# Kernel optimization log

Hardware: AMD Instinct MI355X
Metric: run time of the kernel (lower is better)

The kernel has to match this reference:

```python
import jax, jax.numpy as jnp
import numpy as np

NUM_REL = 7
EPS = 1e-5
N, E = 30000, 480000
D_IN, D_H = 21, 512


def _bn(x, g, b):
    # BatchNorm1d over nodes (training-mode batch statistics, biased var like torch)
    mu = x.mean(axis=0)
    var = x.var(axis=0)
    return (x - mu) * jax.lax.rsqrt(var + EPS) * g + b


def _conv(x, src, seg_idx, lin_w, lin_b, self_w, self_b, bn_g, bn_b):
    # GeometricRelationalGraphConv: gather src features, scatter-add per (dst, relation)
    d = x.shape[1]
    msg = x[src]                                                   # (E, d)
    upd = jax.ops.segment_sum(msg, seg_idx, num_segments=N * NUM_REL)
    upd = upd.reshape(N, NUM_REL * d)                              # (N, 7*d)
    out = upd @ lin_w.T + lin_b + x @ self_w.T + self_b            # linear + self-loop
    out = _bn(out, bn_g, bn_b)                                     # conv-internal BN
    return jax.nn.relu(out)


def setup_inputs() -> dict:
    key = jax.random.key(0)
    ks = jax.random.split(key, 16)
    inp = {
        "x": jax.random.normal(ks[0], (N, D_IN), dtype=jnp.float32),
        "src": jax.random.randint(ks[1], (E,), 0, N, dtype=jnp.int32),
        "dst": jax.random.randint(ks[2], (E,), 0, N, dtype=jnp.int32),
        "rel": jax.random.randint(ks[3], (E,), 0, NUM_REL, dtype=jnp.int32),
    }
    dims = [(D_IN, D_H), (D_H, D_H), (D_H, D_H)]
    k = 4
    for i, (din, dout) in enumerate(dims):
        inp[f"lin_w{i}"] = jax.random.normal(ks[k], (dout, NUM_REL * din), dtype=jnp.float32) * 0.05
        inp[f"self_w{i}"] = jax.random.normal(ks[k + 1], (dout, din), dtype=jnp.float32) * 0.05
        k += 2
        inp[f"lin_b{i}"] = jnp.zeros((dout,), jnp.float32)
        inp[f"self_b{i}"] = jnp.zeros((dout,), jnp.float32)
        inp[f"bn1_g{i}"] = jnp.ones((dout,), jnp.float32)
        inp[f"bn1_b{i}"] = jnp.zeros((dout,), jnp.float32)
        inp[f"bn2_g{i}"] = jnp.ones((dout,), jnp.float32)
        inp[f"bn2_b{i}"] = jnp.zeros((dout,), jnp.float32)
    return inp


def reference(x, src, dst, rel,
              lin_w0, lin_b0, self_w0, self_b0, bn1_g0, bn1_b0, bn2_g0, bn2_b0,
              lin_w1, lin_b1, self_w1, self_b1, bn1_g1, bn1_b1, bn2_g1, bn2_b1,
              lin_w2, lin_b2, self_w2, self_b2, bn1_g2, bn1_b2, bn2_g2, bn2_b2):
    seg_idx = dst * NUM_REL + rel                                  # (E,)
    layers = [
        (lin_w0, lin_b0, self_w0, self_b0, bn1_g0, bn1_b0, bn2_g0, bn2_b0),
        (lin_w1, lin_b1, self_w1, self_b1, bn1_g1, bn1_b1, bn2_g1, bn2_b1),
        (lin_w2, lin_b2, self_w2, self_b2, bn1_g2, bn1_b2, bn2_g2, bn2_b2),
    ]
    hiddens = []
    h = x
    for lw, lb, sw, sb, g1, b1, g2, b2 in layers:
        h = _conv(h, src, seg_idx, lw, lb, sw, sb, g1, b1)
        h = _bn(h, g2, b2)                                         # GearNet outer BN
        hiddens.append(h)
    return jnp.concatenate(hiddens, axis=-1)                      # (N, 3*512) concat_hidden
```

## Files before the change

### kernel.cpp

```cpp
#include <hip/hip_runtime.h>

#define NN   30000
#define NE   480000
#define NR   7
#define NSEG (NN*NR)
#define DH   512
#define DIN  21
#define EPSB 1e-5f
#define BK   32
#define KSEG 3584
#define CHMAX 15360

typedef __attribute__((ext_vector_type(8))) short bf16x8;
typedef __attribute__((ext_vector_type(8))) unsigned short u16x8;
typedef __attribute__((ext_vector_type(4))) float f32x4;
typedef unsigned short ushortT;

static inline size_t align256(size_t x){ return (x + 255) & ~(size_t)255; }

__device__ inline float bf2f(ushortT u){
    unsigned int i = ((unsigned int)u) << 16; float f; __builtin_memcpy(&f, &i, 4); return f;
}
__device__ inline ushortT f2bf(float f){
    unsigned int i; __builtin_memcpy(&i, &f, 4);
    unsigned int r = i + 0x7FFFu + ((i >> 16) & 1u);
    return (ushortT)(r >> 16);
}

__device__ inline void load_lds16(const ushortT* g, ushortT* l){
    __builtin_amdgcn_global_load_lds((const __attribute__((address_space(1))) unsigned int*)g,
                                     (__attribute__((address_space(3))) unsigned int*)l,
                                     16, 0, 0);
}


__global__ void hist_k(const int* __restrict__ dst, const int* __restrict__ rel,
                       int* __restrict__ counts){
    int e = blockIdx.x*256 + threadIdx.x;
    if (e < NE) atomicAdd(&counts[dst[e]*NR + rel[e]], 1);
}

__global__ void scan1_k(const int* __restrict__ counts, int* __restrict__ bsum){
    __shared__ int sd[256];
    int t = threadIdx.x;
    int base = blockIdx.x*1024 + t*4;
    int s = 0;
#pragma unroll
    for (int i = 0; i < 4; i++){ int idx = base + i; if (idx < NSEG) s += counts[idx]; }
    sd[t] = s; __syncthreads();
    for (int off = 128; off > 0; off >>= 1){
        if (t < off) sd[t] += sd[t+off];
        __syncthreads();
    }
    if (t == 0) bsum[blockIdx.x] = sd[0];
}

__global__ void scan2_k(int* __restrict__ bsum, int nb, int* __restrict__ seg_start){
    __shared__ int sd[256];
    int t = threadIdx.x;
    int v = (t < nb) ? bsum[t] : 0;
    sd[t] = v; __syncthreads();
    for (int off = 1; off < 256; off <<= 1){
        int x = sd[t];
        if (t >= off) x += sd[t-off];
        __syncthreads();
        sd[t] = x; __syncthreads();
    }
    if (t < nb) bsum[t] = (t == 0) ? 0 : sd[t-1];
    if (t == 0) seg_start[NSEG] = NE;
}

__global__ void scan3_k(const int* __restrict__ counts, const int* __restrict__ bsum,
                        int* __restrict__ seg_start){
    __shared__ int sd[256];
    int t = threadIdx.x;
    int base = blockIdx.x*1024 + t*4;
    int v[4]; int s = 0;
#pragma unroll
    for (int i = 0; i < 4; i++){ int idx = base + i; v[i] = (idx < NSEG) ? counts[idx] : 0; s += v[i]; }
    sd[t] = s; __syncthreads();
    for (int off = 1; off < 256; off <<= 1){
        int x = sd[t];
        if (t >= off) x += sd[t-off];
        __syncthreads();
        sd[t] = x; __syncthreads();
    }
    int excl = sd[t] - s + bsum[blockIdx.x];
#pragma unroll
    for (int i = 0; i < 4; i++){
        int idx = base + i;
        if (idx < NSEG){ seg_start[idx] = excl; excl += v[i]; }
    }
}

__global__ void scatter_k(const int* __restrict__ src, const int* __restrict__ dst,
                          const int* __restrict__ rel, const int* __restrict__ seg_start,
                          int* __restrict__ cursor, int* __restrict__ src_sorted){
    int e = blockIdx.x*256 + threadIdx.x;
    if (e < NE){
        int s = dst[e]*NR + rel[e];
        int pos = seg_start[s] + atomicAdd(&cursor[s], 1);
        src_sorted[pos] = src[e];
    }
}


__global__ void segsum21b_k(const float* __restrict__ x0,
                            const int* __restrict__ seg_start, const int* __restrict__ src_sorted,
                            ushortT* __restrict__ Acat){
    int n = blockIdx.x;
    int t = threadIdx.x;
    ushortT* arow = Acat + (long)n*192;
    if (t < DIN){
        int sb = n*NR;
        int e0 = seg_start[sb];
#pragma unroll
        for (int r = 0; r < NR; r++){
            int e1 = seg_start[sb + r + 1];
            float a = 0.f;
            for (int e = e0; e < e1; e++) a += x0[(long)src_sorted[e]*DIN + t];
            e0 = e1;
            arow[r*DIN + t] = f2bf(a);
        }
        arow[7*DIN + t] = f2bf(x0[(long)n*DIN + t]);
    }
    if (t >= 40) arow[168 + (t - 40)] = 0;
}


__global__ __launch_bounds__(256)
void segsum_wave_k(const ushortT* __restrict__ hbf,
                   const int* __restrict__ seg_start, const int* __restrict__ src_sorted,
                   ushortT* __restrict__ Acat, int c0, int cn){
    int wid = (blockIdx.x*256 + threadIdx.x) >> 6;
    if (wid >= cn) return;
    const int n = c0 + wid;
    const int lane = (threadIdx.x & 63);
    const int co = lane*8;

    int sb[8];
#pragma unroll
    for (int i = 0; i < 8; i++) sb[i] = seg_start[n*NR + i];

    ushortT* arow = Acat + (long)wid*KSEG + co;
#pragma unroll
    for (int r = 0; r < NR; r++){
        float a[8];
#pragma unroll
        for (int j = 0; j < 8; j++) a[j] = 0.f;
        int e = sb[r], e1 = sb[r+1];
        for (; e + 1 < e1; e += 2){
            u16x8 v0 = *reinterpret_cast<const u16x8*>(hbf + (long)src_sorted[e]*DH + co);
            u16x8 v1 = *reinterpret_cast<const u16x8*>(hbf + (long)src_sorted[e+1]*DH + co);
#pragma unroll
            for (int j = 0; j < 8; j++) a[j] += bf2f((ushortT)v0[j]) + bf2f((ushortT)v1[j]);
        }
        if (e < e1){
            u16x8 v = *reinterpret_cast<const u16x8*>(hbf + (long)src_sorted[e]*DH + co);
#pragma unroll
            for (int j = 0; j < 8; j++) a[j] += bf2f((ushortT)v[j]);
        }
        u16x8 o;
#pragma unroll
        for (int j = 0; j < 8; j++) o[j] = f2bf(a[j]);
        *reinterpret_cast<u16x8*>(arow + r*DH) = o;
    }
}


__global__ void convw_k(const float* __restrict__ lw, const float* __restrict__ sw,
                        int d, int Kp, ushortT* __restrict__ Wc){
    int i = blockIdx.x*256 + threadIdx.x;
    if (i < DH*Kp){
        int n = i / Kp, k = i % Kp;
        float v;
        if (k < 7*d)      v = lw[(long)n*7*d + k];
        else if (k < 8*d) v = sw[(long)n*d + (k - 7*d)];
        else              v = 0.f;
        Wc[i] = f2bf(v);
    }
}


__global__ __launch_bounds__(256)
void gemm_mfma_k(const ushortT* __restrict__ A, int lda, int ntA,
                 const ushortT* __restrict__ hbase, int M,
                 const ushortT* __restrict__ W, int ldw,
                 const float* __restrict__ b1, const float* __restrict__ b2,
                 float* __restrict__ C, int nt, float* __restrict__ sums){
    __shared__ ushortT As[3][128*BK];
    __shared__ ushortT Bs[3][128*BK];
    const int t    = threadIdx.x;

    const int nwg = gridDim.x;
    int q = nwg >> 3, rmd = nwg & 7;
    int xcd = blockIdx.x & 7, slot = blockIdx.x >> 3;
    int l = xcd*q + min(xcd, rmd) + slot;
    const int bm = (l >> 2)*128;
    const int bn = (l & 3)*128;

    const int w    = t >> 6;
    const int lane = t & 63;

    int f0 = w*128 + lane, f1 = f0 + 64;
    const int ar0 = min(bm + (f0 >> 2), M-1), ac0 = (f0 & 3)*8;
    const int ar1 = min(bm + (f1 >> 2), M-1), ac1 = (f1 & 3)*8;
    const int br0 = bn + (f0 >> 2), br1 = bn + (f1 >> 2);
    const int d0 = (w*128 +  0)*8;
    const int d1 = (w*128 + 64)*8;

    f32x4 acc[4][4];
#pragma unroll
    for (int m = 0; m < 4; m++)
#pragma unroll
        for (int n = 0; n < 4; n++) acc[m][n] = (f32x4){0.f,0.f,0.f,0.f};

    const int wm = w >> 1, wn = w & 1;
    const int r = lane & 15, hi = lane >> 4;

    auto stage = [&](int kt, int b){
        const ushortT* p0;
        const ushortT* p1;
        if (kt < ntA){
            p0 = A + (long)ar0*lda + kt*BK + ac0;
            p1 = A + (long)ar1*lda + kt*BK + ac1;
        } else {
            int k0 = (kt - ntA)*BK;
            p0 = hbase + (long)ar0*DH + k0 + ac0;
            p1 = hbase + (long)ar1*DH + k0 + ac1;
        }
        load_lds16(p0, &As[b][d0]);
        load_lds16(p1, &As[b][d1]);
        load_lds16(W + (long)br0*ldw + kt*BK + ac0, &Bs[b][d0]);
        load_lds16(W + (long)br1*ldw + kt*BK + ac1, &Bs[b][d1]);
    };

    stage(0, 0);
    stage(1, 1);

    for (int kt = 0; kt < nt; ++kt){
        if (kt + 1 < nt) asm volatile("s_waitcnt vmcnt(4)" ::: "memory");
        else             asm volatile("s_waitcnt vmcnt(0)" ::: "memory");
        __builtin_amdgcn_s_barrier();
        __builtin_amdgcn_sched_barrier(0);
        if (kt + 2 < nt) stage(kt + 2, (kt + 2) % 3);
        const int buf = kt % 3;
        bf16x8 af[4], bfr[4];
#pragma unroll
        for (int m = 0; m < 4; m++)
            af[m] = *reinterpret_cast<const bf16x8*>(&As[buf][(wm*64 + m*16 + r)*BK + hi*8]);
#pragma unroll
        for (int n = 0; n < 4; n++)
            bfr[n] = *reinterpret_cast<const bf16x8*>(&Bs[buf][(wn*64 + n*16 + r)*BK + hi*8]);
#pragma unroll
        for (int m = 0; m < 4; m++)
#pragma unroll
            for (int n = 0; n < 4; n++)
                acc[m][n] = __builtin_amdgcn_mfma_f32_16x16x32_bf16(af[m], bfr[n], acc[m][n], 0, 0, 0);
    }

#pragma unroll
    for (int n = 0; n < 4; n++){
        int col = bn + wn*64 + n*16 + r;
        float bb = b1[col] + b2[col];
        float s = 0.f, s2 = 0.f;
#pragma unroll
        for (int m = 0; m < 4; m++){
            int row = bm + wm*64 + m*16 + hi*4;
#pragma unroll
            for (int q2 = 0; q2 < 4; q2++){
                if (row + q2 < M){
                    float v = acc[m][n][q2] + bb;
                    C[(long)(row + q2)*DH + col] = v;
                    s += v; s2 = fmaf(v, v, s2);
                }
            }
        }
        s  += __shfl_xor(s, 16);  s  += __shfl_xor(s, 32);
        s2 += __shfl_xor(s2, 16); s2 += __shfl_xor(s2, 32);
        if (hi == 0){
            atomicAdd(&sums[col], s);
            atomicAdd(&sums[DH + col], s2);
        }
    }
}


__global__ void finalize_k(const float* __restrict__ sums, const float* __restrict__ g,
                           const float* __restrict__ b, float* __restrict__ ac){
    int c = blockIdx.x*256 + threadIdx.x;
    if (c < DH){
        float mu  = sums[c] * (1.f/NN);
        float var = sums[DH + c] * (1.f/NN) - mu*mu;
        var = fmaxf(var, 0.f);
        float a = g[c] * rsqrtf(var + EPSB);
        ac[c]      = a;
        ac[DH + c] = fmaf(-mu, a, b[c]);
    }
}

__global__ void bnrelu_k(float* __restrict__ buf, int M, const float* __restrict__ ac,
                         float* __restrict__ sums2){
    int col = blockIdx.x*256 + threadIdx.x;
    int r0 = blockIdx.y*128;
    int r1 = min(r0 + 128, M);
    float a = ac[col], c = ac[DH + col];
    float s = 0.f, s2 = 0.f;
    for (int r = r0; r < r1; r++){
        long idx = (long)r*DH + col;
        float y = fmaxf(fmaf(a, buf[idx], c), 0.f);
        buf[idx] = y;
        s += y; s2 = fmaf(y, y, s2);
    }
    atomicAdd(&sums2[col], s);
    atomicAdd(&sums2[DH + col], s2);
}

__global__ void bn2write_k(const float* __restrict__ buf, const float* __restrict__ ac,
                           float* __restrict__ out, ushortT* __restrict__ hbf, int layer){
    long i = (long)blockIdx.x*256 + threadIdx.x;
    if (i < (long)NN*DH){
        int r = (int)(i >> 9);
        int c = (int)(i & 511);
        float h = fmaf(ac[c], buf[i], ac[DH + c]);
        out[(long)r*(3*DH) + layer*DH + c] = h;
        hbf[i] = f2bf(h);
    }
}


extern "C" void kernel_launch(void* const* d_in, const int* in_sizes, int n_in,
                              void* d_out, int out_size, void* d_ws, size_t ws_size,
                              hipStream_t stream){
    const float* x0  = (const float*)d_in[0];
    const int*   src = (const int*)d_in[1];
    const int*   dst = (const int*)d_in[2];
    const int*   rel = (const int*)d_in[3];
    const float* lin_w[3]  = {(const float*)d_in[4],  (const float*)d_in[12], (const float*)d_in[20]};
    const float* self_w[3] = {(const float*)d_in[5],  (const float*)d_in[13], (const float*)d_in[21]};
    const float* lin_b[3]  = {(const float*)d_in[6],  (const float*)d_in[14], (const float*)d_in[22]};
    const float* self_b[3] = {(const float*)d_in[7],  (const float*)d_in[15], (const float*)d_in[23]};
    const float* bn1_g[3]  = {(const float*)d_in[8],  (const float*)d_in[16], (const float*)d_in[24]};
    const float* bn1_b[3]  = {(const float*)d_in[9],  (const float*)d_in[17], (const float*)d_in[25]};
    const float* bn2_g[3]  = {(const float*)d_in[10], (const float*)d_in[18], (const float*)d_in[26]};
    const float* bn2_b[3]  = {(const float*)d_in[11], (const float*)d_in[19], (const float*)d_in[27]};

    char* ws = (char*)d_ws;
    size_t off = 0;
    auto alloc = [&](size_t bytes)->char*{ char* p = ws + off; off = align256(off + bytes); return p; };

    int*     counts     = (int*)alloc((size_t)NSEG*4);
    int*     cursor     = (int*)alloc((size_t)NSEG*4);
    int*     seg_start  = (int*)alloc((size_t)(NSEG+1)*4);
    int*     bsum       = (int*)alloc(1024*4);
    int*     src_sorted = (int*)alloc((size_t)NE*4);
    float*   stats      = (float*)alloc((size_t)8*DH*4);
    float*   sums1 = stats;            float* sums2 = stats + 2*DH;
    float*   ac1   = stats + 4*DH;     float* ac2   = stats + 6*DH;
    float*   outbuf = (float*)alloc((size_t)NN*DH*4);
    ushortT* hbf    = (ushortT*)alloc((size_t)NN*DH*2);
    ushortT* Wcat   = (ushortT*)alloc((size_t)DH*4096*2);
    ushortT* Acat0  = (ushortT*)alloc((size_t)NN*192*2);

    size_t remain = (ws_size > off) ? (ws_size - off) : 0;
    long max_nodes = (long)(remain / ((size_t)KSEG*2));
    int chunk = (int)((max_nodes > CHMAX) ? CHMAX : max_nodes);
    chunk &= ~127;
    if (chunk < 128) chunk = 128;
    ushortT* Acat = (ushortT*)(ws + off);

    hipMemsetAsync(counts, 0, (size_t)NSEG*4, stream);
    hipMemsetAsync(cursor, 0, (size_t)NSEG*4, stream);
    hist_k<<<(NE+255)/256, 256, 0, stream>>>(dst, rel, counts);
    int nb = (NSEG + 1023)/1024;
    scan1_k<<<nb, 256, 0, stream>>>(counts, bsum);
    scan2_k<<<1, 256, 0, stream>>>(bsum, nb, seg_start);
    scan3_k<<<nb, 256, 0, stream>>>(counts, bsum, seg_start);
    scatter_k<<<(NE+255)/256, 256, 0, stream>>>(src, dst, rel, seg_start, cursor, src_sorted);

    const int MB = (NN + 127)/128;

    for (int layer = 0; layer < 3; layer++){
        int d  = (layer == 0) ? DIN : DH;
        int Kp = (layer == 0) ? 192 : 8*DH;
        convw_k<<<(DH*Kp + 255)/256, 256, 0, stream>>>(lin_w[layer], self_w[layer], d, Kp, Wcat);
        hipMemsetAsync(stats, 0, (size_t)4*DH*4, stream);

        if (layer == 0){
            segsum21b_k<<<NN, 64, 0, stream>>>(x0, seg_start, src_sorted, Acat0);
            gemm_mfma_k<<<MB*4, 256, 0, stream>>>(
                Acat0, 192, 6, Acat0, NN, Wcat, 192,
                lin_b[layer], self_b[layer], outbuf, 6, sums1);
        } else {
            for (int c0 = 0; c0 < NN; c0 += chunk){
                int cn = (NN - c0 < chunk) ? (NN - c0) : chunk;
                segsum_wave_k<<<(cn + 3)/4, 256, 0, stream>>>(
                    hbf, seg_start, src_sorted, Acat, c0, cn);
                gemm_mfma_k<<<((cn + 127)/128)*4, 256, 0, stream>>>(
                    Acat, KSEG, 112, hbf + (long)c0*DH, cn, Wcat, 4096,
                    lin_b[layer], self_b[layer],
                    outbuf + (long)c0*DH, 128, sums1);
            }
        }

        finalize_k<<<2, 256, 0, stream>>>(sums1, bn1_g[layer], bn1_b[layer], ac1);
        bnrelu_k<<<dim3(2, (NN+127)/128), 256, 0, stream>>>(outbuf, NN, ac1, sums2);
        finalize_k<<<2, 256, 0, stream>>>(sums2, bn2_g[layer], bn2_b[layer], ac2);
        bn2write_k<<<((long)NN*DH + 255)/256, 256, 0, stream>>>(outbuf, ac2, (float*)d_out, hbf, layer);
    }
}
```

Baseline: 959.5 us.

## Overlap next-chunk segment sum with GEMM in a merged kernel, narrow GEMM tile

```diff
diff --git a/kernel.cpp b/kernel.cpp
--- a/kernel.cpp
+++ b/kernel.cpp
@@ -128,43 +128,54 @@
 }
 
 
+__device__ inline void segsum_body(const ushortT* __restrict__ hbf,
+                                   const int* __restrict__ seg_start,
+                                   const int* __restrict__ src_sorted,
+                                   ushortT* __restrict__ Acat,
+                                   int wid, int c0, int lane){
+    const int n = c0 + wid;
+    const int co = lane*8;
+
+    int sb[8];
+#pragma unroll
+    for (int i = 0; i < 8; i++) sb[i] = seg_start[n*NR + i];
+
+    ushortT* arow = Acat + (long)wid*KSEG + co;
+#pragma unroll
+    for (int r = 0; r < NR; r++){
+        float a[8];
+#pragma unroll
+        for (int j = 0; j < 8; j++) a[j] = 0.f;
+        int e = sb[r], e1 = sb[r+1];
+        for (; e + 3 < e1; e += 4){
+            u16x8 v0 = *reinterpret_cast<const u16x8*>(hbf + (long)src_sorted[e  ]*DH + co);
+            u16x8 v1 = *reinterpret_cast<const u16x8*>(hbf + (long)src_sorted[e+1]*DH + co);
+            u16x8 v2 = *reinterpret_cast<const u16x8*>(hbf + (long)src_sorted[e+2]*DH + co);
+            u16x8 v3 = *reinterpret_cast<const u16x8*>(hbf + (long)src_sorted[e+3]*DH + co);
+#pragma unroll
+            for (int j = 0; j < 8; j++)
+                a[j] += (bf2f((ushortT)v0[j]) + bf2f((ushortT)v1[j]))
+                      + (bf2f((ushortT)v2[j]) + bf2f((ushortT)v3[j]));
+        }
+        for (; e < e1; e++){
+            u16x8 v = *reinterpret_cast<const u16x8*>(hbf + (long)src_sorted[e]*DH + co);
+#pragma unroll
+            for (int j = 0; j < 8; j++) a[j] += bf2f((ushortT)v[j]);
+        }
+        u16x8 o;
+#pragma unroll
+        for (int j = 0; j < 8; j++) o[j] = f2bf(a[j]);
+        *reinterpret_cast<u16x8*>(arow + r*DH) = o;
+    }
+}
+
 __global__ __launch_bounds__(256)
 void segsum_wave_k(const ushortT* __restrict__ hbf,
                    const int* __restrict__ seg_start, const int* __restrict__ src_sorted,
                    ushortT* __restrict__ Acat, int c0, int cn){
     int wid = (blockIdx.x*256 + threadIdx.x) >> 6;
     if (wid >= cn) return;
-    const int n = c0 + wid;
-    const int lane = (threadIdx.x & 63);
-    const int co = lane*8;
-
-    int sb[8];
-#pragma unroll
-    for (int i = 0; i < 8; i++) sb[i] = seg_start[n*NR + i];
-
-    ushortT* arow = Acat + (long)wid*KSEG + co;
-#pragma unroll
-    for (int r = 0; r < NR; r++){
-        float a[8];
-#pragma unroll
-        for (int j = 0; j < 8; j++) a[j] = 0.f;
-        int e = sb[r], e1 = sb[r+1];
-        for (; e + 1 < e1; e += 2){
-            u16x8 v0 = *reinterpret_cast<const u16x8*>(hbf + (long)src_sorted[e]*DH + co);
-            u16x8 v1 = *reinterpret_cast<const u16x8*>(hbf + (long)src_sorted[e+1]*DH + co);
-#pragma unroll
-            for (int j = 0; j < 8; j++) a[j] += bf2f((ushortT)v0[j]) + bf2f((ushortT)v1[j]);
-        }
-        if (e < e1){
-            u16x8 v = *reinterpret_cast<const u16x8*>(hbf + (long)src_sorted[e]*DH + co);
-#pragma unroll
-            for (int j = 0; j < 8; j++) a[j] += bf2f((ushortT)v[j]);
-        }
-        u16x8 o;
-#pragma unroll
-        for (int j = 0; j < 8; j++) o[j] = f2bf(a[j]);
-        *reinterpret_cast<u16x8*>(arow + r*DH) = o;
-    }
+    segsum_body(hbf, seg_start, src_sorted, Acat, wid, c0, threadIdx.x & 63);
 }
 
 
@@ -183,38 +194,46 @@
 
 
 __global__ __launch_bounds__(256)
-void gemm_mfma_k(const ushortT* __restrict__ A, int lda, int ntA,
-                 const ushortT* __restrict__ hbase, int M,
-                 const ushortT* __restrict__ W, int ldw,
-                 const float* __restrict__ b1, const float* __restrict__ b2,
-                 float* __restrict__ C, int nt, float* __restrict__ sums){
+void gemm_seg_k(int gemmBlocks,
+                const ushortT* __restrict__ A, int lda, int ntA,
+                const ushortT* __restrict__ hbase, int M,
+                const ushortT* __restrict__ W, int ldw,
+                const float* __restrict__ b1, const float* __restrict__ b2,
+                float* __restrict__ C, int nt, float* __restrict__ sums,
+                const ushortT* __restrict__ hbf,
+                const int* __restrict__ seg_start, const int* __restrict__ src_sorted,
+                ushortT* __restrict__ Acat2, int nc0, int ncn){
     __shared__ ushortT As[3][128*BK];
-    __shared__ ushortT Bs[3][128*BK];
-    const int t    = threadIdx.x;
-
-    const int nwg = gridDim.x;
+    __shared__ ushortT Bs[3][ 64*BK];
+    const int t = threadIdx.x;
+
+    if ((int)blockIdx.x >= gemmBlocks){
+        int wid = ((int)blockIdx.x - gemmBlocks)*4 + (t >> 6);
+        if (wid < ncn)
+            segsum_body(hbf, seg_start, src_sorted, Acat2, wid, nc0, t & 63);
+        return;
+    }
+
+    const int nwg = gemmBlocks;
     int q = nwg >> 3, rmd = nwg & 7;
     int xcd = blockIdx.x & 7, slot = blockIdx.x >> 3;
     int l = xcd*q + min(xcd, rmd) + slot;
-    const int bm = (l >> 2)*128;
-    const int bn = (l & 3)*128;
-
-    const int w    = t >> 6;
+    const int bm = (l >> 3)*128;
+    const int bn = (l & 7)*64;
+
+    const int ar0 = min(bm + (t >> 2), M-1);
+    const int ar1 = min(bm + 64 + (t >> 2), M-1);
+    const int acu = (t & 3)*8;
+    const int brw = bn + (t >> 2);
+
+    f32x4 acc[4][2];
+#pragma unroll
+    for (int m = 0; m < 4; m++)
+#pragma unroll
+        for (int n = 0; n < 2; n++) acc[m][n] = (f32x4){0.f,0.f,0.f,0.f};
+
+    const int w = t >> 6;
     const int lane = t & 63;
-
-    int f0 = w*128 + lane, f1 = f0 + 64;
-    const int ar0 = min(bm + (f0 >> 2), M-1), ac0 = (f0 & 3)*8;
-    const int ar1 = min(bm + (f1 >> 2), M-1), ac1 = (f1 & 3)*8;
-    const int br0 = bn + (f0 >> 2), br1 = bn + (f1 >> 2);
-    const int d0 = (w*128 +  0)*8;
-    const int d1 = (w*128 + 64)*8;
-
-    f32x4 acc[4][4];
-#pragma unroll
-    for (int m = 0; m < 4; m++)
-#pragma unroll
-        for (int n = 0; n < 4; n++) acc[m][n] = (f32x4){0.f,0.f,0.f,0.f};
-
     const int wm = w >> 1, wn = w & 1;
     const int r = lane & 15, hi = lane >> 4;
 
@@ -222,46 +241,45 @@
         const ushortT* p0;
         const ushortT* p1;
         if (kt < ntA){
-            p0 = A + (long)ar0*lda + kt*BK + ac0;
-            p1 = A + (long)ar1*lda + kt*BK + ac1;
+            p0 = A + (long)ar0*lda + kt*BK + acu;
+            p1 = A + (long)ar1*lda + kt*BK + acu;
         } else {
             int k0 = (kt - ntA)*BK;
-            p0 = hbase + (long)ar0*DH + k0 + ac0;
-            p1 = hbase + (long)ar1*DH + k0 + ac1;
-        }
-        load_lds16(p0, &As[b][d0]);
-        load_lds16(p1, &As[b][d1]);
-        load_lds16(W + (long)br0*ldw + kt*BK + ac0, &Bs[b][d0]);
-        load_lds16(W + (long)br1*ldw + kt*BK + ac1, &Bs[b][d1]);
+            p0 = hbase + (long)ar0*DH + k0 + acu;
+            p1 = hbase + (long)ar1*DH + k0 + acu;
+        }
+        load_lds16(p0, &As[b][t*8]);
+        load_lds16(p1, &As[b][(t + 256)*8]);
+        load_lds16(W + (long)brw*ldw + kt*BK + acu, &Bs[b][t*8]);
     };
 
     stage(0, 0);
     stage(1, 1);
 
     for (int kt = 0; kt < nt; ++kt){
-        if (kt + 1 < nt) asm volatile("s_waitcnt vmcnt(4)" ::: "memory");
+        if (kt + 1 < nt) asm volatile("s_waitcnt vmcnt(3)" ::: "memory");
         else             asm volatile("s_waitcnt vmcnt(0)" ::: "memory");
         __builtin_amdgcn_s_barrier();
         __builtin_amdgcn_sched_barrier(0);
         if (kt + 2 < nt) stage(kt + 2, (kt + 2) % 3);
         const int buf = kt % 3;
-        bf16x8 af[4], bfr[4];
+        bf16x8 af[4], bfr[2];
 #pragma unroll
         for (int m = 0; m < 4; m++)
             af[m] = *reinterpret_cast<const bf16x8*>(&As[buf][(wm*64 + m*16 + r)*BK + hi*8]);
 #pragma unroll
-        for (int n = 0; n < 4; n++)
-            bfr[n] = *reinterpret_cast<const bf16x8*>(&Bs[buf][(wn*64 + n*16 + r)*BK + hi*8]);
+        for (int n = 0; n < 2; n++)
+            bfr[n] = *reinterpret_cast<const bf16x8*>(&Bs[buf][(wn*32 + n*16 + r)*BK + hi*8]);
 #pragma unroll
         for (int m = 0; m < 4; m++)
 #pragma unroll
-            for (int n = 0; n < 4; n++)
+            for (int n = 0; n < 2; n++)
                 acc[m][n] = __builtin_amdgcn_mfma_f32_16x16x32_bf16(af[m], bfr[n], acc[m][n], 0, 0, 0);
     }
 
 #pragma unroll
-    for (int n = 0; n < 4; n++){
-        int col = bn + wn*64 + n*16 + r;
+    for (int n = 0; n < 2; n++){
+        int col = bn + wn*32 + n*16 + r;
         float bb = b1[col] + b2[col];
         float s = 0.f, s2 = 0.f;
 #pragma unroll
@@ -363,11 +381,13 @@
     ushortT* Acat0  = (ushortT*)alloc((size_t)NN*192*2);
 
     size_t remain = (ws_size > off) ? (ws_size - off) : 0;
-    long max_nodes = (long)(remain / ((size_t)KSEG*2));
+    long max_nodes = (long)(remain / (2*(size_t)KSEG*2));
     int chunk = (int)((max_nodes > CHMAX) ? CHMAX : max_nodes);
     chunk &= ~127;
     if (chunk < 128) chunk = 128;
-    ushortT* Acat = (ushortT*)(ws + off);
+    ushortT* AcatA = (ushortT*)(ws + off);
+    ushortT* AcatB = AcatA + (size_t)chunk*KSEG;
+    ushortT* AcatBuf[2] = {AcatA, AcatB};
 
     hipMemsetAsync(counts, 0, (size_t)NSEG*4, stream);
     hipMemsetAsync(cursor, 0, (size_t)NSEG*4, stream);
@@ -379,6 +399,7 @@
     scatter_k<<<(NE+255)/256, 256, 0, stream>>>(src, dst, rel, seg_start, cursor, src_sorted);
 
     const int MB = (NN + 127)/128;
+    const int nch = (NN + chunk - 1)/chunk;
 
     for (int layer = 0; layer < 3; layer++){
         int d  = (layer == 0) ? DIN : DH;
@@ -388,18 +409,31 @@
 
         if (layer == 0){
             segsum21b_k<<<NN, 64, 0, stream>>>(x0, seg_start, src_sorted, Acat0);
-            gemm_mfma_k<<<MB*4, 256, 0, stream>>>(
-                Acat0, 192, 6, Acat0, NN, Wcat, 192,
-                lin_b[layer], self_b[layer], outbuf, 6, sums1);
+            gemm_seg_k<<<MB*8, 256, 0, stream>>>(
+                MB*8, Acat0, 192, 6, Acat0, NN, Wcat, 192,
+                lin_b[layer], self_b[layer], outbuf, 6, sums1,
+                hbf, seg_start, src_sorted, (ushortT*)nullptr, 0, 0);
         } else {
-            for (int c0 = 0; c0 < NN; c0 += chunk){
-                int cn = (NN - c0 < chunk) ? (NN - c0) : chunk;
-                segsum_wave_k<<<(cn + 3)/4, 256, 0, stream>>>(
-                    hbf, seg_start, src_sorted, Acat, c0, cn);
-                gemm_mfma_k<<<((cn + 127)/128)*4, 256, 0, stream>>>(
-                    Acat, KSEG, 112, hbf + (long)c0*DH, cn, Wcat, 4096,
-                    lin_b[layer], self_b[layer],
-                    outbuf + (long)c0*DH, 128, sums1);
+            int cn0 = (NN < chunk) ? NN : chunk;
+            segsum_wave_k<<<(cn0 + 3)/4, 256, 0, stream>>>(
+                hbf, seg_start, src_sorted, AcatBuf[0], 0, cn0);
+            for (int i = 0; i < nch; i++){
+                int cc0 = i*chunk;
+                int ccn = (NN - cc0 < chunk) ? (NN - cc0) : chunk;
+                int gemmBlocks = ((ccn + 127)/128)*8;
+                int segBlocks = 0, nc0 = 0, ncn = 0;
+                ushortT* An = nullptr;
+                if (i + 1 < nch){
+                    nc0 = (i + 1)*chunk;
+                    ncn = (NN - nc0 < chunk) ? (NN - nc0) : chunk;
+                    segBlocks = (ncn + 3)/4;
+                    An = AcatBuf[(i + 1) & 1];
+                }
+                gemm_seg_k<<<gemmBlocks + segBlocks, 256, 0, stream>>>(
+                    gemmBlocks, AcatBuf[i & 1], KSEG, 112, hbf + (long)cc0*DH, ccn,
+                    Wcat, 4096, lin_b[layer], self_b[layer],
+                    outbuf + (long)cc0*DH, 128, sums1,
+                    hbf, seg_start, src_sorted, An, nc0, ncn);
             }
         }
 
```

Measured after the change: 1.040 ms. +8.4%, slower.
